# Kernel tuning notes

Hardware: AMD Instinct MI355X
Metric: run time of the kernel (lower is better)

The kernel has to match this reference:

```python
import jax, jax.numpy as jnp
import numpy as np
import math

H = 16  # n_heads


def setup_inputs() -> dict:
    key = jax.random.key(0)
    ks = jax.random.split(key, 12)
    B, S, D = 8, 1024, 1024
    inp = {
        "query": jax.random.normal(ks[0], (B, S, D), jnp.float32),
        "key_": jax.random.normal(ks[1], (B, S, D), jnp.float32),
        "value": jax.random.normal(ks[2], (B, S, D), jnp.float32),
        "mask": jnp.ones((B, S, S), jnp.int32),
        "attn_pos": jax.random.normal(ks[3], (1, H, S, S), jnp.float32),
    }
    sc = 1.0 / math.sqrt(D)
    for i, nm in enumerate(["q", "k", "v", "o"]):
        inp[f"w{nm}"] = jax.random.normal(ks[4 + i], (D, D), jnp.float32) * sc
        inp[f"b{nm}"] = jax.random.normal(ks[8 + i], (D,), jnp.float32) * 0.01
    return inp


def reference(query, key_, value, mask, attn_pos, wq, bq, wk, bk, wv, bv, wo, bo):
    B, S, D = query.shape
    dk = D // H

    def proj(x, w, b):  # [B,S,D] -> [B,H,S,dk]
        return (x @ w.T + b).reshape(B, S, H, dk).transpose(0, 2, 1, 3)

    q = proj(query, wq, bq)
    k = proj(key_, wk, bk)
    v = proj(value, wv, bv)

    # attn_pos branch: scale by sqrt(2*d_k), add positional bias
    scores = jnp.einsum("bhqd,bhkd->bhqk", q, k) / math.sqrt(2 * dk) + attn_pos
    scores = jnp.where(mask[:, None] == 0, -1e9, scores)
    p = jax.nn.softmax(scores, axis=-1)  # dropout inactive (eval)
    x = jnp.einsum("bhqk,bhkd->bhqd", p, v)
    x = x.transpose(0, 2, 1, 3).reshape(B, S, D)
    x = x @ wo.T + bo          # linears[-1] applied once...
    return x @ wo.T + bo       # ...and again, faithful to source
```

## Files before the change

### kernel.cpp

```cpp
#include <hip/hip_runtime.h>
#include <hip/hip_bf16.h>

typedef unsigned short u16;
typedef unsigned int u32;
typedef __attribute__((ext_vector_type(8))) short bfrag;
typedef __attribute__((ext_vector_type(4))) float f32x4;

#define DEVINL __device__ __forceinline__

DEVINL u16 f2bf(float f) {
  u32 u = __float_as_uint(f);
  u32 r = (u + 0x7fffu + ((u >> 16) & 1u)) >> 16;
  return (u16)r;
}
DEVINL float bf2f(u16 u) { return __uint_as_float(((u32)u) << 16); }
DEVINL u32 cvtpk(float lo, float hi) {
  u32 r;
  asm("v_cvt_pk_bf16_f32 %0, %1, %2" : "=v"(r) : "v"(lo), "v"(hi));
  return r;
}
DEVINL u16 f2bf_hw(float v) { return (u16)cvtpk(v, v); }
DEVINL float fmax3(float a, float b, float c) { return fmaxf(fmaxf(a, b), c); }

DEVINL void gload_lds16(const void* g, void* l) {
  __builtin_amdgcn_global_load_lds(
      (const __attribute__((address_space(1))) void*)g,
      (__attribute__((address_space(3))) void*)l, 16, 0, 0);
}

DEVINL void storeC(u16* C, size_t idx, float v) { C[idx] = f2bf_hw(v); }
DEVINL void storeC(float* C, size_t idx, float v) { C[idx] = v; }

#define SBAR0 __builtin_amdgcn_sched_barrier(0)

DEVINL void gemm_decode(int gid, int& m0, int& n0) {
  const int m = ((gid >> 6) << 3) | (gid & 7);
  const int n = (gid >> 3) & 7;
  m0 = m * 128;
  n0 = n * 128;
}


__global__ void cast_w4(const float* __restrict__ w0, const float* __restrict__ w1,
                        const float* __restrict__ w2, const float* __restrict__ w3,
                        u16* __restrict__ o0, u16* __restrict__ o1,
                        u16* __restrict__ o2, u16* __restrict__ o3) {
  const int which = blockIdx.x >> 10;
  const int i = (blockIdx.x & 1023) * 256 + threadIdx.x;
  const float* in = which == 0 ? w0 : which == 1 ? w1 : which == 2 ? w2 : w3;
  u16* out = which == 0 ? o0 : which == 1 ? o1 : which == 2 ? o2 : o3;
  const float4 f = ((const float4*)in)[i];
  uint2 r;
  r.x = cvtpk(f.x, f.y);
  r.y = cvtpk(f.z, f.w);
  ((uint2*)out)[i] = r;
}

__global__ void pack_mask(const int* __restrict__ mask, u32* __restrict__ bits) {
  const size_t wi = (size_t)blockIdx.x * 256 + threadIdx.x;
  const int* src = mask + wi * 32;
  u32 v = 0;
#pragma unroll
  for (int i = 0; i < 8; ++i) {
    const int4 m4 = ((const int4*)src)[i];
    if (m4.x) v |= 1u << (i * 4 + 0);
    if (m4.y) v |= 1u << (i * 4 + 1);
    if (m4.z) v |= 1u << (i * 4 + 2);
    if (m4.w) v |= 1u << (i * 4 + 3);
  }
  bits[wi] = v;
}

__global__ void transpose_cast(const float* __restrict__ in, u16* __restrict__ out) {
  __shared__ u16 tile[64][65];
  const int t = threadIdx.x;
  const int bx = blockIdx.x, by = blockIdx.y;
#pragma unroll
  for (int p = 0; p < 4; ++p) {
    const int r = (t >> 4) + p * 16;
    const int c = (t & 15) * 4;
    const float4 f = *(const float4*)&in[(size_t)(by * 64 + r) * 1024 + bx * 64 + c];
    tile[c + 0][r] = f2bf(f.x);
    tile[c + 1][r] = f2bf(f.y);
    tile[c + 2][r] = f2bf(f.z);
    tile[c + 3][r] = f2bf(f.w);
  }
  __syncthreads();
#pragma unroll
  for (int p = 0; p < 4; ++p) {
    const int r = (t >> 4) + p * 16;
    const int c = (t & 15) * 4;
    uint2 v;
    v.x = (u32)tile[r][c] | ((u32)tile[r][c + 1] << 16);
    v.y = (u32)tile[r][c + 2] | ((u32)tile[r][c + 3] << 16);
    *(uint2*)&out[(size_t)(bx * 64 + r) * 1024 + by * 64 + c] = v;
  }
}

__global__ void bias2(const float* __restrict__ wo, const float* __restrict__ bo,
                      float* __restrict__ bo2) {
  const int w = threadIdx.x >> 6, lane = threadIdx.x & 63;
  const int row = blockIdx.x * 4 + w;
  const float* src = wo + (size_t)row * 1024;
  float s = 0.f;
#pragma unroll
  for (int i = 0; i < 4; ++i) {
    const float4 f = *(const float4*)&src[lane * 4 + i * 256];
    const float4 g = *(const float4*)&bo[lane * 4 + i * 256];
    s += f.x * g.x + f.y * g.y + f.z * g.z + f.w * g.w;
  }
#pragma unroll
  for (int d = 1; d < 64; d <<= 1) s += __shfl_xor(s, d);
  if (lane == 0) bo2[row] = s + bo[row];
}

__global__ __launch_bounds__(256) void gemm_bt_64(
    const u16* __restrict__ A, const u16* __restrict__ W,
    u16* __restrict__ C, int N, int K) {
  __shared__ u16 sA[64 * 64];
  __shared__ u16 sB[64 * 64];
  const int t = threadIdx.x;
  const int w = t >> 6, lane = t & 63;
  const int lr = lane & 15, lk = (lane >> 4) * 8;
  const int m0 = blockIdx.x * 64, n0 = blockIdx.y * 64;
  f32x4 acc[4] = {};
  for (int k0 = 0; k0 < K; k0 += 64) {
#pragma unroll
    for (int i = 0; i < 2; ++i) {
      const int idx = i * 256 + t;
      const int row = idx >> 3;
      const int col = (idx & 7) * 8;
      gload_lds16(A + (size_t)(m0 + row) * K + k0 + col, &sA[idx * 8]);
      gload_lds16(W + (size_t)(n0 + row) * K + k0 + col, &sB[idx * 8]);
    }
    __syncthreads();
#pragma unroll
    for (int ks = 0; ks < 2; ++ks) {
      const bfrag av = *(const bfrag*)&sA[(w * 16 + lr) * 64 + ks * 32 + lk];
#pragma unroll
      for (int n = 0; n < 4; ++n) {
        const bfrag bv = *(const bfrag*)&sB[(n * 16 + lr) * 64 + ks * 32 + lk];
        acc[n] = __builtin_amdgcn_mfma_f32_16x16x32_bf16(av, bv, acc[n], 0, 0, 0);
      }
    }
    __syncthreads();
  }
  const int orow = (lane >> 4) * 4;
#pragma unroll
  for (int n = 0; n < 4; ++n)
#pragma unroll
    for (int j = 0; j < 4; ++j)
      C[(size_t)(m0 + w * 16 + orow + j) * N + n0 + n * 16 + lr] = f2bf_hw(acc[n][j]);
}


__global__ __launch_bounds__(256) void gemm_qkv(
    const float* __restrict__ Aq, const float* __restrict__ Ak, const float* __restrict__ Av,
    const u16* __restrict__ Wq, const u16* __restrict__ Wk, const u16* __restrict__ Wv,
    const float* __restrict__ Bq, const float* __restrict__ Bk, const float* __restrict__ Bv,
    u16* __restrict__ Qb, u16* __restrict__ Kb, u16* __restrict__ Vt, float qs) {
  __shared__ __align__(16) u16 sA[128 * 64];
  __shared__ __align__(16) u16 sB[128 * 64];
  const int gid = blockIdx.x;
  const int which = gid >> 9;
  int m0, n0;
  gemm_decode(gid & 511, m0, n0);
  const float* A = which == 0 ? Aq : which == 1 ? Ak : Av;
  const u16* W = which == 0 ? Wq : which == 1 ? Wk : Wv;
  const float* bias = which == 0 ? Bq : which == 1 ? Bk : Bv;
  const int t = threadIdx.x;
  const int w = t >> 6, lane = t & 63;
  const int lr = lane & 15, lg = lane >> 4;
  const int wr = (w >> 1) * 64, wc = (w & 1) * 64;
  f32x4 acc[4][4] = {};

  for (int kt = 0; kt < 16; ++kt) {
    const int k0 = kt * 64;
    f32x4 fa[4][2];
#pragma unroll
    for (int i = 0; i < 4; ++i) {
      const int idx = i * 256 + t;
      const int row = idx >> 3;
      const int cg = idx & 7;
      const float* src = A + (size_t)(m0 + row) * 1024 + k0 + cg * 8;
      fa[i][0] = *(const f32x4*)src;
      fa[i][1] = *(const f32x4*)(src + 4);
    }
    if (kt) __syncthreads();
#pragma unroll
    for (int i = 0; i < 4; ++i) {
      const int idx = i * 256 + t;
      const int row = idx >> 3;
      const int cg = idx & 7;
      uint4 pk;
      pk.x = cvtpk(fa[i][0][0], fa[i][0][1]);
      pk.y = cvtpk(fa[i][0][2], fa[i][0][3]);
      pk.z = cvtpk(fa[i][1][0], fa[i][1][1]);
      pk.w = cvtpk(fa[i][1][2], fa[i][1][3]);
      *(uint4*)((char*)sA + row * 128 + ((cg ^ (row & 7)) * 16)) = pk;
      gload_lds16(W + (size_t)(n0 + row) * 1024 + k0 + ((cg ^ (row & 7)) * 8),
                  (char*)sB + idx * 16);
    }
    __syncthreads();
#pragma unroll
    for (int ks = 0; ks < 2; ++ks) {
      bfrag av[4], bv[4];
#pragma unroll
      for (int m = 0; m < 4; ++m) {
        const int row = wr + m * 16 + lr;
        av[m] = *(const bfrag*)((const char*)sA + row * 128 + ((ks * 64 + lg * 16) ^ ((row & 7) << 4)));
      }
#pragma unroll
      for (int n = 0; n < 4; ++n) {
        const int row = wc + n * 16 + lr;
        bv[n] = *(const bfrag*)((const char*)sB + row * 128 + ((ks * 64 + lg * 16) ^ ((row & 7) << 4)));
      }
#pragma unroll
      for (int m = 0; m < 4; ++m)
#pragma unroll
        for (int n = 0; n < 4; ++n)
          acc[m][n] = __builtin_amdgcn_mfma_f32_16x16x32_bf16(av[m], bv[n], acc[m][n], 0, 0, 0);
    }
  }

  float bz[4];
#pragma unroll
  for (int n = 0; n < 4; ++n) bz[n] = bias[n0 + wc + n * 16 + lr];
  const int orow = lg * 4;
  if (which == 2) {
#pragma unroll
    for (int m = 0; m < 4; ++m) {
#pragma unroll
      for (int n = 0; n < 4; ++n) {
        const int r0 = m0 + wr + m * 16 + orow;
        const int c = n0 + wc + n * 16 + lr;
        const int bb = r0 >> 10, s = r0 & 1023;
        const int h = c >> 6, d = c & 63;
        uint2 v;
        v.x = cvtpk(acc[m][n][0] + bz[n], acc[m][n][1] + bz[n]);
        v.y = cvtpk(acc[m][n][2] + bz[n], acc[m][n][3] + bz[n]);
        *(uint2*)&Vt[(((size_t)bb * 16 + h) * 64 + d) * 1024 + s] = v;
      }
    }
  } else {
    u16* C = which == 0 ? Qb : Kb;
    const float osc = which == 0 ? qs : 1.0f;
#pragma unroll
    for (int m = 0; m < 4; ++m) {
#pragma unroll
      for (int n = 0; n < 4; ++n) {
        const int r = m0 + wr + m * 16 + orow;
        const int c = n0 + wc + n * 16 + lr;
#pragma unroll
        for (int j = 0; j < 4; ++j)
          C[(size_t)(r + j) * 1024 + c] = f2bf_hw((acc[m][n][j] + bz[n]) * osc);
      }
    }
  }
}


template <typename OutT>
__global__ __launch_bounds__(256) void gemm_bt_a16(
    const u16* __restrict__ A, const u16* __restrict__ W,
    const float* __restrict__ bias, OutT* __restrict__ C,
    int M, int N, int K) {
  __shared__ __align__(16) u16 sA[2][128 * 64];
  __shared__ __align__(16) u16 sB[2][128 * 64];
  const int t = threadIdx.x;
  const int w = t >> 6, lane = t & 63;
  const int lr = lane & 15, lg = lane >> 4;
  int m0, n0;
  gemm_decode(blockIdx.x, m0, n0);
  const int wr = (w >> 1) * 64, wc = (w & 1) * 64;
  f32x4 acc[4][4] = {};
  const int nk = K >> 6;

#pragma unroll
  for (int i = 0; i < 4; ++i) {
    const int idx = i * 256 + t;
    const int row = idx >> 3;
    const int col = ((idx & 7) ^ (row & 7)) * 8;
    gload_lds16(A + (size_t)(m0 + row) * K + col, (char*)sA[0] + idx * 16);
    gload_lds16(W + (size_t)(n0 + row) * K + col, (char*)sB[0] + idx * 16);
  }
  SBAR0; asm volatile("s_waitcnt vmcnt(0)" ::: "memory"); SBAR0;
  __builtin_amdgcn_s_barrier(); SBAR0;

#pragma unroll 2
  for (int kt = 0; kt < nk; ++kt) {
    const int cur = kt & 1;
    if (kt < nk - 1) {
      const int k0 = (kt + 1) * 64;
#pragma unroll
      for (int i = 0; i < 4; ++i) {
        const int idx = i * 256 + t;
        const int row = idx >> 3;
        const int col = ((idx & 7) ^ (row & 7)) * 8;
        gload_lds16(A + (size_t)(m0 + row) * K + k0 + col, (char*)sA[cur ^ 1] + idx * 16);
        gload_lds16(W + (size_t)(n0 + row) * K + k0 + col, (char*)sB[cur ^ 1] + idx * 16);
      }
    }
    const char* pA = (const char*)sA[cur];
    const char* pB = (const char*)sB[cur];
#pragma unroll
    for (int ks = 0; ks < 2; ++ks) {
      bfrag av[4], bv[4];
#pragma unroll
      for (int m = 0; m < 4; ++m) {
        const int row = wr + m * 16 + lr;
        av[m] = *(const bfrag*)(pA + row * 128 + ((ks * 64 + lg * 16) ^ ((row & 7) << 4)));
      }
#pragma unroll
      for (int n = 0; n < 4; ++n) {
        const int row = wc + n * 16 + lr;
        bv[n] = *(const bfrag*)(pB + row * 128 + ((ks * 64 + lg * 16) ^ ((row & 7) << 4)));
      }
#pragma unroll
      for (int m = 0; m < 4; ++m)
#pragma unroll
        for (int n = 0; n < 4; ++n)
          acc[m][n] = __builtin_amdgcn_mfma_f32_16x16x32_bf16(av[m], bv[n], acc[m][n], 0, 0, 0);
    }
    if (kt < nk - 1) {
      SBAR0; asm volatile("s_waitcnt vmcnt(0)" ::: "memory"); SBAR0;
      __builtin_amdgcn_s_barrier(); SBAR0;
    }
  }

  float bz[4];
#pragma unroll
  for (int n = 0; n < 4; ++n) bz[n] = bias[n0 + wc + n * 16 + lr];
  const int orow = lg * 4;
#pragma unroll
  for (int m = 0; m < 4; ++m) {
#pragma unroll
    for (int n = 0; n < 4; ++n) {
      const int r = m0 + wr + m * 16 + orow;
      const int c = n0 + wc + n * 16 + lr;
#pragma unroll
      for (int j = 0; j < 4; ++j)
        storeC(C, (size_t)(r + j) * N + c, acc[m][n][j] + bz[n]);
    }
  }
}


__global__ __launch_bounds__(512, 4) void attn_fwd(
    const u16* __restrict__ Qm, const u16* __restrict__ Km,
    const u16* __restrict__ Vt, const float* __restrict__ pos,
    const u32* __restrict__ mbits, u16* __restrict__ Om) {
  const int gid = blockIdx.x;
  const int h = (gid & 7) + 8 * (gid >> 9);
  const int inner = (gid >> 3) & 63;
  const int bb = inner & 7;
  const int qt = inner >> 3;
  const int t = threadIdx.x;
  const int w = t >> 6, lane = t & 63;
  const int lr = lane & 15, lg = lane >> 4;
  const float log2e = 1.4426950408889634f;

  __shared__ __align__(16) char smem[49152];

  const int q0 = qt * 128;
  const size_t baseQ = ((size_t)bb * 1024) * 1024 + (size_t)h * 64;
  const size_t baseV = ((size_t)(bb * 16 + h) * 64) * 1024;
  const int qg = q0 + w * 16 + lr;
  const float* posrow = pos + ((size_t)h * 1024 + qg) * 1024;
  const u32* mrow = mbits + ((size_t)bb * 1024 + qg) * 32;

#pragma unroll
  for (int i = 0; i < 2; ++i) {
    const int idx = i * 512 + t;
    const int r = idx >> 3;
    const int w8 = idx & 7;
    gload_lds16(Qm + baseQ + (size_t)(q0 + r) * 1024 + (w8 ^ (r & 7)) * 8, smem + idx * 16);
  }
  {
    const int r = t >> 3;
    const int w8 = t & 7;
    gload_lds16(Km + baseQ + (size_t)r * 1024 + (w8 ^ (r & 7)) * 8, smem + 16384 + t * 16);
    gload_lds16(Vt + baseV + (size_t)r * 1024 + (w8 ^ (r & 7)) * 8, smem + 24576 + t * 16);
  }

  u32 ok = 0xffffffffu;
#pragma unroll
  for (int i = 0; i < 8; ++i) {
    const uint4 m4 = *(const uint4*)&mrow[i * 4];
    ok &= m4.x & m4.y & m4.z & m4.w;
  }
  const bool allone = __all(ok == 0xffffffffu);

  float4 pz[4];
#pragma unroll
  for (int n = 0; n < 4; ++n) pz[n] = *(const float4*)&posrow[n * 16 + lg * 4];

  __syncthreads();

  bfrag qv[2];
#pragma unroll
  for (int ks = 0; ks < 2; ++ks) {
    const int byt = (w * 16 + lr) * 128 + ((ks * 64 + lg * 16) ^ ((lr & 7) << 4));
    qv[ks] = *(const bfrag*)(smem + byt);
  }
  __syncthreads();

  f32x4 o[4] = {};
  float m_q = -3.0e38f, l_q = 0.f;

  for (int kt = 0; kt < 16; ++kt) {
    const int cur = kt & 1;
    const char* sK = smem + (cur ? 0 : 16384);
    const char* sV = smem + (cur ? 8192 : 24576);

    float4 pzn[4];
    if (kt < 15) {
      const int kn = (kt + 1) * 64;
      char* dK = smem + (cur ? 16384 : 0);
      char* dV = smem + (cur ? 24576 : 8192);
      const int r = t >> 3;
      const int w8 = t & 7;
      gload_lds16(Km + baseQ + (size_t)(kn + r) * 1024 + (w8 ^ (r & 7)) * 8, dK + t * 16);
      gload_lds16(Vt + baseV + (size_t)r * 1024 + kn + (w8 ^ (r & 7)) * 8, dV + t * 16);
#pragma unroll
      for (int n = 0; n < 4; ++n) pzn[n] = *(const float4*)&posrow[kn + n * 16 + lg * 4];
    }

    f32x4 s[4] = {};
    __builtin_amdgcn_s_setprio(1);
#pragma unroll
    for (int ks = 0; ks < 2; ++ks) {
#pragma unroll
      for (int n = 0; n < 4; ++n) {
        const int byt = (n * 16 + lr) * 128 + ((ks * 64 + lg * 16) ^ ((lr & 7) << 4));
        const bfrag kf = *(const bfrag*)(sK + byt);
        s[n] = __builtin_amdgcn_mfma_f32_16x16x32_bf16(kf, qv[ks], s[n], 0, 0, 0);
      }
    }
    __builtin_amdgcn_s_setprio(0);

    float pv[16];
#pragma unroll
    for (int n = 0; n < 4; ++n) {
      pv[n * 4 + 0] = fmaf(pz[n].x, log2e, s[n][0]);
      pv[n * 4 + 1] = fmaf(pz[n].y, log2e, s[n][1]);
      pv[n * 4 + 2] = fmaf(pz[n].z, log2e, s[n][2]);
      pv[n * 4 + 3] = fmaf(pz[n].w, log2e, s[n][3]);
    }

    if (!allone) {
      const u32 a0 = mrow[kt * 2], a1 = mrow[kt * 2 + 1];
#pragma unroll
      for (int n = 0; n < 4; ++n)
#pragma unroll
        for (int j = 0; j < 4; ++j) {
          const int kl = n * 16 + lg * 4 + j;
          const u32 mw = (kl & 32) ? a1 : a0;
          if (!((mw >> (kl & 31)) & 1u)) pv[n * 4 + j] = -1.0e9f;
        }
    }

    float tmax = fmax3(pv[0], pv[1], pv[2]);
    tmax = fmax3(tmax, pv[3], pv[4]);
    tmax = fmax3(tmax, pv[5], pv[6]);
    tmax = fmax3(tmax, pv[7], pv[8]);
    tmax = fmax3(tmax, pv[9], pv[10]);
    tmax = fmax3(tmax, pv[11], pv[12]);
    tmax = fmax3(tmax, pv[13], pv[14]);
    tmax = fmaxf(tmax, pv[15]);
    tmax = fmaxf(tmax, __shfl_xor(tmax, 16));
    tmax = fmaxf(tmax, __shfl_xor(tmax, 32));

    if (!__all(tmax <= m_q + 8.0f)) {
      const float mn = fmaxf(m_q, tmax);
      const float sc = __builtin_amdgcn_exp2f(m_q - mn);
      l_q *= sc;
#pragma unroll
      for (int j = 0; j < 4; ++j) {
        const float scj = __shfl(sc, lg * 4 + j);
#pragma unroll
        for (int n = 0; n < 4; ++n) o[n][j] *= scj;
      }
      m_q = mn;
    }
    float rs = 0.f;
#pragma unroll
    for (int i2 = 0; i2 < 16; ++i2) {
      pv[i2] = __builtin_amdgcn_exp2f(pv[i2] - m_q);
      rs += pv[i2];
    }
    rs += __shfl_xor(rs, 16);
    rs += __shfl_xor(rs, 32);
    l_q += rs;

    char* pbuf = smem + 32768 + w * 2048;
#pragma unroll
    for (int n = 0; n < 4; ++n) {
      uint2 pk;
      pk.x = cvtpk(pv[n * 4 + 0], pv[n * 4 + 1]);
      pk.y = cvtpk(pv[n * 4 + 2], pv[n * 4 + 3]);
      const int byt = lr * 128 + ((n * 32 + lg * 8) ^ ((lr & 7) << 4));
      *(uint2*)(pbuf + byt) = pk;
    }
    __builtin_amdgcn_s_setprio(1);
#pragma unroll
    for (int ks = 0; ks < 2; ++ks) {
      const int pbyt = lr * 128 + ((ks * 64 + lg * 16) ^ ((lr & 7) << 4));
      const bfrag pf = *(const bfrag*)(pbuf + pbyt);
#pragma unroll
      for (int n = 0; n < 4; ++n) {
        const int vb = (n * 16 + lr) * 128 + ((ks * 64 + lg * 16) ^ ((lr & 7) << 4));
        const bfrag vf = *(const bfrag*)(sV + vb);
        o[n] = __builtin_amdgcn_mfma_f32_16x16x32_bf16(pf, vf, o[n], 0, 0, 0);
      }
    }
    __builtin_amdgcn_s_setprio(0);

    __syncthreads();

    if (kt < 15) {
#pragma unroll
      for (int n = 0; n < 4; ++n) pz[n] = pzn[n];
    }
  }

#pragma unroll
  for (int j = 0; j < 4; ++j) {
    const float lj = __shfl(l_q, lg * 4 + j);
    const float inv = 1.f / lj;
    const int qr = q0 + w * 16 + lg * 4 + j;
#pragma unroll
    for (int n = 0; n < 4; ++n)
      Om[baseQ + (size_t)qr * 1024 + n * 16 + lr] = f2bf_hw(o[n][j] * inv);
  }
}


extern "C" void kernel_launch(void* const* d_in, const int* in_sizes, int n_in,
                              void* d_out, int out_size, void* d_ws, size_t ws_size,
                              hipStream_t stream) {
  const float* query = (const float*)d_in[0];
  const float* key_  = (const float*)d_in[1];
  const float* value = (const float*)d_in[2];
  const int*   mask  = (const int*)d_in[3];
  const float* pos   = (const float*)d_in[4];
  const float* wq = (const float*)d_in[5];
  const float* bq = (const float*)d_in[6];
  const float* wk = (const float*)d_in[7];
  const float* bk = (const float*)d_in[8];
  const float* wv = (const float*)d_in[9];
  const float* bv = (const float*)d_in[10];
  const float* wo = (const float*)d_in[11];
  const float* bo = (const float*)d_in[12];

  char* ws = (char*)d_ws;
  const size_t MB = 1024 * 1024;
  u16* wqb  = (u16*)(ws + 0 * MB);
  u16* wkb  = (u16*)(ws + 2 * MB);
  u16* wvb  = (u16*)(ws + 4 * MB);
  u16* wob  = (u16*)(ws + 6 * MB);
  u16* Qb   = (u16*)(ws + 40 * MB);
  u16* Kb   = (u16*)(ws + 56 * MB);
  u16* Vtb  = (u16*)(ws + 72 * MB);
  u16* Xa   = (u16*)(ws + 88 * MB);
  u32* mb   = (u32*)(ws + 104 * MB);
  u16* wotb = (u16*)(ws + 105 * MB);
  u16* W2b  = (u16*)(ws + 107 * MB);
  float* bo2 = (float*)(ws + 109 * MB);

  const float log2e = 1.4426950408889634f;
  const float qs = 0.0883883476483184f * log2e;

  cast_w4<<<4096, 256, 0, stream>>>(wq, wk, wv, wo, wqb, wkb, wvb, wob);
  pack_mask<<<1024, 256, 0, stream>>>(mask, mb);
  transpose_cast<<<dim3(16, 16), 256, 0, stream>>>(wo, wotb);
  bias2<<<256, 256, 0, stream>>>(wo, bo, bo2);

  gemm_bt_64<<<dim3(16, 16), 256, 0, stream>>>(wob, wotb, W2b, 1024, 1024);

  gemm_qkv<<<1536, 256, 0, stream>>>(query, key_, value, wqb, wkb, wvb,
                                     bq, bk, bv, Qb, Kb, Vtb, qs);

  attn_fwd<<<1024, 512, 0, stream>>>(Qb, Kb, Vtb, pos, mb, Xa);

  gemm_bt_a16<float><<<512, 256, 0, stream>>>(Xa, W2b, bo2, (float*)d_out, 8192, 1024, 1024);
}
```

Measured before the change: 229.0 us.

## Software-pipeline QKV GEMM with register-prefetched A and double-buffered B tiles

Restructures the QKV projection GEMM main loop so the next K-tile of fp32 activations is prefetched into registers and the next weight tile is loaded asynchronously into a second LDS buffer while the current tile is multiplied. Explicit vmcnt waits and raw barriers replace __syncthreads. The aim is to hide global-load latency behind MFMA work. In exchange it uses more registers and LDS, which could lower occupancy, and it depends on the vmcnt count matching the number of outstanding loads.

```diff
diff --git a/kernel.cpp b/kernel.cpp
--- a/kernel.cpp
+++ b/kernel.cpp
@@ -160,7 +160,7 @@
     const float* __restrict__ Bq, const float* __restrict__ Bk, const float* __restrict__ Bv,
     u16* __restrict__ Qb, u16* __restrict__ Kb, u16* __restrict__ Vt, float qs) {
   __shared__ __align__(16) u16 sA[128 * 64];
-  __shared__ __align__(16) u16 sB[128 * 64];
+  __shared__ __align__(16) u16 sB[2][128 * 64];
   const int gid = blockIdx.x;
   const int which = gid >> 9;
   int m0, n0;
@@ -174,34 +174,59 @@
   const int wr = (w >> 1) * 64, wc = (w & 1) * 64;
   f32x4 acc[4][4] = {};
 
+  const int srow = t >> 3;
+  const int scg = t & 7;
+
+  f32x4 fa_cur[4][2], fa_next[4][2];
+#pragma unroll
+  for (int i = 0; i < 4; ++i) {
+    const int row = srow + i * 32;
+    const float* src = A + (size_t)(m0 + row) * 1024 + scg * 8;
+    fa_cur[i][0] = *(const f32x4*)src;
+    fa_cur[i][1] = *(const f32x4*)(src + 4);
+  }
+#pragma unroll
+  for (int i = 0; i < 4; ++i) {
+    const int row = srow + i * 32;
+    gload_lds16(W + (size_t)(n0 + row) * 1024 + ((scg ^ (row & 7)) * 8),
+                (char*)sB[0] + (i * 256 + t) * 16);
+  }
+
+#pragma unroll 2
   for (int kt = 0; kt < 16; ++kt) {
-    const int k0 = kt * 64;
-    f32x4 fa[4][2];
+    const int cur = kt & 1;
+    if (kt < 15) {
+      const int k1 = (kt + 1) * 64;
+#pragma unroll
+      for (int i = 0; i < 4; ++i) {
+        const int row = srow + i * 32;
+        const float* src = A + (size_t)(m0 + row) * 1024 + k1 + scg * 8;
+        fa_next[i][0] = *(const f32x4*)src;
+        fa_next[i][1] = *(const f32x4*)(src + 4);
+      }
+#pragma unroll
+      for (int i = 0; i < 4; ++i) {
+        const int row = srow + i * 32;
+        gload_lds16(W + (size_t)(n0 + row) * 1024 + k1 + ((scg ^ (row & 7)) * 8),
+                    (char*)sB[cur ^ 1] + (i * 256 + t) * 16);
+      }
+    }
 #pragma unroll
     for (int i = 0; i < 4; ++i) {
-      const int idx = i * 256 + t;
-      const int row = idx >> 3;
-      const int cg = idx & 7;
-      const float* src = A + (size_t)(m0 + row) * 1024 + k0 + cg * 8;
-      fa[i][0] = *(const f32x4*)src;
-      fa[i][1] = *(const f32x4*)(src + 4);
-    }
-    if (kt) __syncthreads();
-#pragma unroll
-    for (int i = 0; i < 4; ++i) {
-      const int idx = i * 256 + t;
-      const int row = idx >> 3;
-      const int cg = idx & 7;
+      const int row = srow + i * 32;
       uint4 pk;
-      pk.x = cvtpk(fa[i][0][0], fa[i][0][1]);
-      pk.y = cvtpk(fa[i][0][2], fa[i][0][3]);
-      pk.z = cvtpk(fa[i][1][0], fa[i][1][1]);
-      pk.w = cvtpk(fa[i][1][2], fa[i][1][3]);
-      *(uint4*)((char*)sA + row * 128 + ((cg ^ (row & 7)) * 16)) = pk;
-      gload_lds16(W + (size_t)(n0 + row) * 1024 + k0 + ((cg ^ (row & 7)) * 8),
-                  (char*)sB + idx * 16);
-    }
-    __syncthreads();
+      pk.x = cvtpk(fa_cur[i][0][0], fa_cur[i][0][1]);
+      pk.y = cvtpk(fa_cur[i][0][2], fa_cur[i][0][3]);
+      pk.z = cvtpk(fa_cur[i][1][0], fa_cur[i][1][1]);
+      pk.w = cvtpk(fa_cur[i][1][2], fa_cur[i][1][3]);
+      *(uint4*)((char*)sA + row * 128 + ((scg ^ (row & 7)) * 16)) = pk;
+    }
+    SBAR0;
+    if (kt < 15) asm volatile("s_waitcnt vmcnt(12) lgkmcnt(0)" ::: "memory");
+    else         asm volatile("s_waitcnt vmcnt(0) lgkmcnt(0)" ::: "memory");
+    SBAR0;
+    __builtin_amdgcn_s_barrier(); SBAR0;
+
 #pragma unroll
     for (int ks = 0; ks < 2; ++ks) {
       bfrag av[4], bv[4];
@@ -213,13 +238,21 @@
 #pragma unroll
       for (int n = 0; n < 4; ++n) {
         const int row = wc + n * 16 + lr;
-        bv[n] = *(const bfrag*)((const char*)sB + row * 128 + ((ks * 64 + lg * 16) ^ ((row & 7) << 4)));
+        bv[n] = *(const bfrag*)((const char*)sB[cur] + row * 128 + ((ks * 64 + lg * 16) ^ ((row & 7) << 4)));
       }
 #pragma unroll
       for (int m = 0; m < 4; ++m)
 #pragma unroll
         for (int n = 0; n < 4; ++n)
           acc[m][n] = __builtin_amdgcn_mfma_f32_16x16x32_bf16(av[m], bv[n], acc[m][n], 0, 0, 0);
+    }
+    if (kt < 15) {
+      __builtin_amdgcn_s_barrier(); SBAR0;
+#pragma unroll
+      for (int i = 0; i < 4; ++i) {
+        fa_cur[i][0] = fa_next[i][0];
+        fa_cur[i][1] = fa_next[i][1];
+      }
     }
   }
 
```

Result: slower. 245.8 us (+7.3%).

## Prefetch next fp32 A tile into registers during current K-step in QKV GEMM

Applied to the files above, without the earlier changes.

Restructures the QKV projection GEMM main loop to software-pipeline the fp32 activation loads. The next K-tile of A is loaded into registers while the current tile's MFMAs run. Explicit s_barrier and partial vmcnt waits replace __syncthreads so the outstanding prefetch loads are not drained before compute. This hides global load latency at the cost of hand-managed wait counts, which must exactly match the number of in-flight loads to stay correct.

```diff
diff --git a/kernel.cpp b/kernel.cpp
--- a/kernel.cpp
+++ b/kernel.cpp
@@ -174,34 +174,58 @@
   const int wr = (w >> 1) * 64, wc = (w & 1) * 64;
   f32x4 acc[4][4] = {};
 
+  const int srow = t >> 3;
+  const int scg = t & 7;
+
+  f32x4 fa[4][2];
+#pragma unroll
+  for (int i = 0; i < 4; ++i) {
+    const int row = srow + i * 32;
+    const float* src = A + (size_t)(m0 + row) * 1024 + scg * 8;
+    fa[i][0] = *(const f32x4*)src;
+    fa[i][1] = *(const f32x4*)(src + 4);
+  }
+
   for (int kt = 0; kt < 16; ++kt) {
-    const int k0 = kt * 64;
-    f32x4 fa[4][2];
+    if (kt) { __builtin_amdgcn_s_barrier(); SBAR0; }
+
 #pragma unroll
     for (int i = 0; i < 4; ++i) {
-      const int idx = i * 256 + t;
-      const int row = idx >> 3;
-      const int cg = idx & 7;
-      const float* src = A + (size_t)(m0 + row) * 1024 + k0 + cg * 8;
-      fa[i][0] = *(const f32x4*)src;
-      fa[i][1] = *(const f32x4*)(src + 4);
-    }
-    if (kt) __syncthreads();
-#pragma unroll
-    for (int i = 0; i < 4; ++i) {
-      const int idx = i * 256 + t;
-      const int row = idx >> 3;
-      const int cg = idx & 7;
+      const int row = srow + i * 32;
       uint4 pk;
       pk.x = cvtpk(fa[i][0][0], fa[i][0][1]);
       pk.y = cvtpk(fa[i][0][2], fa[i][0][3]);
       pk.z = cvtpk(fa[i][1][0], fa[i][1][1]);
       pk.w = cvtpk(fa[i][1][2], fa[i][1][3]);
-      *(uint4*)((char*)sA + row * 128 + ((cg ^ (row & 7)) * 16)) = pk;
-      gload_lds16(W + (size_t)(n0 + row) * 1024 + k0 + ((cg ^ (row & 7)) * 8),
-                  (char*)sB + idx * 16);
-    }
-    __syncthreads();
+      *(uint4*)((char*)sA + row * 128 + ((scg ^ (row & 7)) * 16)) = pk;
+    }
+    SBAR0;
+    {
+      const int k0 = kt * 64;
+#pragma unroll
+      for (int i = 0; i < 4; ++i) {
+        const int row = srow + i * 32;
+        gload_lds16(W + (size_t)(n0 + row) * 1024 + k0 + ((scg ^ (row & 7)) * 8),
+                    (char*)sB + (i * 256 + t) * 16);
+      }
+    }
+    SBAR0;
+    if (kt < 15) {
+      const int k1 = (kt + 1) * 64;
+#pragma unroll
+      for (int i = 0; i < 4; ++i) {
+        const int row = srow + i * 32;
+        const float* src = A + (size_t)(m0 + row) * 1024 + k1 + scg * 8;
+        fa[i][0] = *(const f32x4*)src;
+        fa[i][1] = *(const f32x4*)(src + 4);
+      }
+    }
+    SBAR0;
+    if (kt < 15) asm volatile("s_waitcnt vmcnt(8) lgkmcnt(0)" ::: "memory");
+    else         asm volatile("s_waitcnt vmcnt(0) lgkmcnt(0)" ::: "memory");
+    SBAR0;
+    __builtin_amdgcn_s_barrier(); SBAR0;
+
 #pragma unroll
     for (int ks = 0; ks < 2; ++ks) {
       bfrag av[4], bv[4];
```

Result: slower. 235.3 us (+2.8%).
